# Optimization experiments

Hardware: AMD Instinct MI355X
Metric: run time of the kernel (lower is better)

Reference implementation:

```python
import jax, jax.numpy as jnp
import numpy as np

N_HEAD = 16
D_MODEL = 1024
D_HEAD = D_MODEL // N_HEAD  # 64
B, S = 1, 4096


def setup_inputs() -> dict:
    key = jax.random.key(0)
    ks = jax.random.split(key, 7)
    q = jax.random.normal(ks[0], (B, S, D_MODEL), dtype=jnp.float32)
    k = jax.random.normal(ks[1], (B, S, D_MODEL), dtype=jnp.float32)
    v = jax.random.normal(ks[2], (B, S, D_MODEL), dtype=jnp.float32)
    mask = jnp.ones((S, S), dtype=bool)
    # params match torch.rand init (uniform [0,1)); use uniform here too
    w_q = jax.random.uniform(ks[3], (D_MODEL, D_MODEL), dtype=jnp.float32)
    w_k = jax.random.uniform(ks[4], (D_HEAD, D_MODEL), dtype=jnp.float32)
    w_v = jax.random.uniform(ks[5], (D_HEAD, D_MODEL), dtype=jnp.float32)
    w_out = jax.random.uniform(ks[6], (D_MODEL, D_MODEL), dtype=jnp.float32)
    return {"q": q, "k": k, "v": v, "mask": mask,
            "w_q": w_q, "w_k": w_k, "w_v": w_v, "w_out": w_out}


def reference(q, k, v, mask, w_q, w_k, w_v, w_out):
    # F.linear(x, W) == x @ W.T
    query = q @ w_q.T                      # [b, n, d_model]
    key = k @ w_k.T                        # [b, s, d_head]  (single shared KV head)
    value = v @ w_v.T                      # [b, s, d_head]
    b, n, _ = query.shape
    query = query.reshape(b, n, N_HEAD, D_HEAD).transpose(0, 2, 1, 3)  # b h n d
    scores = jnp.einsum('bhnd,bsd->bhns', query, key) / jnp.sqrt(jnp.float32(D_HEAD))
    scores = jnp.where(mask[None, None], scores, jnp.float32(-jnp.inf))
    attn = jax.nn.softmax(scores, axis=-1)             # [b, h, n, s]
    out = jnp.einsum('bhns,bsd->bhnd', attn, value)    # [b, h, n, d]
    out = out.transpose(0, 2, 1, 3).reshape(b, n, D_MODEL)
    return out @ w_out.T
```

## Files before the change

### kernel.cpp

```cpp
#include <hip/hip_runtime.h>
#include <cstdint>
#include <cstddef>

#define S_LEN   4096
#define DM      1024
#define NHEAD   16
#define DH      64

typedef short bf16x8 __attribute__((ext_vector_type(8)));
typedef _Float16 f16x8 __attribute__((ext_vector_type(8)));
typedef float f32x4  __attribute__((ext_vector_type(4)));

__device__ __forceinline__ unsigned short f2bf(float x) {
    uint32_t u = __float_as_uint(x);
    u += 0x7fffu + ((u >> 16) & 1u);
    return (unsigned short)(u >> 16);
}
__device__ __forceinline__ float bf2f(unsigned short u) {
    return __uint_as_float(((uint32_t)u) << 16);
}
__device__ __forceinline__ unsigned short f2h(float x) {
    _Float16 h = (_Float16)x;
    return __builtin_bit_cast(unsigned short, h);
}
__device__ __forceinline__ unsigned pack_h2(float a, float b) {
    return __builtin_bit_cast(unsigned, __builtin_amdgcn_cvt_pkrtz(a, b));
}
__device__ __forceinline__ void gl_lds16(const unsigned short* g, unsigned short* l) {
    __builtin_amdgcn_global_load_lds(
        (const __attribute__((address_space(1))) unsigned int*)g,
        (__attribute__((address_space(3))) unsigned int*)l, 16, 0, 0);
}
__device__ __forceinline__ void split8(const float4& a0, const float4& a1,
                                       ushort4& h0, ushort4& h1,
                                       ushort4& l0, ushort4& l1) {
    h0.x = f2bf(a0.x); l0.x = f2bf(a0.x - bf2f(h0.x));
    h0.y = f2bf(a0.y); l0.y = f2bf(a0.y - bf2f(h0.y));
    h0.z = f2bf(a0.z); l0.z = f2bf(a0.z - bf2f(h0.z));
    h0.w = f2bf(a0.w); l0.w = f2bf(a0.w - bf2f(h0.w));
    h1.x = f2bf(a1.x); l1.x = f2bf(a1.x - bf2f(h1.x));
    h1.y = f2bf(a1.y); l1.y = f2bf(a1.y - bf2f(h1.y));
    h1.z = f2bf(a1.z); l1.z = f2bf(a1.z - bf2f(h1.z));
    h1.w = f2bf(a1.w); l1.w = f2bf(a1.w - bf2f(h1.w));
}

__launch_bounds__(256)
__global__ void pre_kernel(const float* __restrict__ kin, const float* __restrict__ vin,
                           const float* __restrict__ wk, const float* __restrict__ wv,
                           const float* __restrict__ q, const float* __restrict__ wq,
                           const float* __restrict__ wo,
                           unsigned short* __restrict__ Kf, unsigned short* __restrict__ Vtf,
                           unsigned short* __restrict__ qh, unsigned short* __restrict__ ql,
                           unsigned short* __restrict__ wqh, unsigned short* __restrict__ wql,
                           unsigned short* __restrict__ woh)
{
    __shared__ unsigned short As_h[64][72];
    __shared__ unsigned short Bs_h[64][72];
    __shared__ unsigned short As_l[64][72];
    __shared__ unsigned short Bs_l[64][72];

    const int tid = threadIdx.x;
    const int bx  = blockIdx.x;

    if (bx >= 128) {
        const int G1 = 1048576, GW = 262144;
        int i = (bx - 128) * 256 + tid;
        const float* src; unsigned short* h; unsigned short* l = nullptr; int off;
        if (i < G1)            { src = q;  h = qh;  l = ql;  off = i; }
        else if (i < G1 + GW)  { src = wq; h = wqh; l = wql; off = i - G1; }
        else                   { src = wo; h = woh;          off = i - G1 - GW; }
        float4 vv = reinterpret_cast<const float4*>(src)[off];
        ushort4 hh;
        hh.x = f2bf(vv.x); hh.y = f2bf(vv.y); hh.z = f2bf(vv.z); hh.w = f2bf(vv.w);
        reinterpret_cast<ushort4*>(h)[off] = hh;
        if (l) {
            ushort4 ll;
            ll.x = f2bf(vv.x - bf2f(hh.x)); ll.y = f2bf(vv.y - bf2f(hh.y));
            ll.z = f2bf(vv.z - bf2f(hh.z)); ll.w = f2bf(vv.w - bf2f(hh.w));
            reinterpret_cast<ushort4*>(l)[off] = ll;
        }
        return;
    }

    const int wave = tid >> 6;
    const int lane = tid & 63;
    const int lm   = lane & 15;
    const int quad = lane >> 4;
    const bool isK = (bx < 64);
    const int m0   = (bx & 63) * 64;
    const float* A = isK ? kin : vin;
    const float* B = isK ? wk : wv;

    f32x4 acc[4] = {};

    for (int kc = 0; kc < DM; kc += 64) {
        __syncthreads();
#pragma unroll
        for (int i = 0; i < 2; ++i) {
            int c   = tid + i * 256;
            int r   = c >> 3;
            int col = (c & 7) * 8;
            float4 a0 = *(const float4*)&A[(size_t)(m0 + r) * DM + kc + col];
            float4 a1 = *(const float4*)&A[(size_t)(m0 + r) * DM + kc + col + 4];
            float4 b0 = *(const float4*)&B[(size_t)r * DM + kc + col];
            float4 b1 = *(const float4*)&B[(size_t)r * DM + kc + col + 4];
            ushort4 h0, h1, l0, l1;
            split8(a0, a1, h0, h1, l0, l1);
            *(ushort4*)&As_h[r][col] = h0;  *(ushort4*)&As_h[r][col + 4] = h1;
            if (isK) { *(ushort4*)&As_l[r][col] = l0;  *(ushort4*)&As_l[r][col + 4] = l1; }
            split8(b0, b1, h0, h1, l0, l1);
            *(ushort4*)&Bs_h[r][col] = h0;  *(ushort4*)&Bs_h[r][col + 4] = h1;
            if (isK) { *(ushort4*)&Bs_l[r][col] = l0;  *(ushort4*)&Bs_l[r][col + 4] = l1; }
        }
        __syncthreads();
#pragma unroll
        for (int kk = 0; kk < 64; kk += 32) {
            bf16x8 bh = *(const bf16x8*)&Bs_h[wave * 16 + lm][kk + quad * 8];
            bf16x8 bl;
            if (isK) bl = *(const bf16x8*)&Bs_l[wave * 16 + lm][kk + quad * 8];
#pragma unroll
            for (int ms = 0; ms < 4; ++ms) {
                bf16x8 ah = *(const bf16x8*)&As_h[ms * 16 + lm][kk + quad * 8];
                acc[ms] = __builtin_amdgcn_mfma_f32_16x16x32_bf16(ah, bh, acc[ms], 0, 0, 0);
                if (isK) {
                    bf16x8 al = *(const bf16x8*)&As_l[ms * 16 + lm][kk + quad * 8];
                    acc[ms] = __builtin_amdgcn_mfma_f32_16x16x32_bf16(ah, bl, acc[ms], 0, 0, 0);
                    acc[ms] = __builtin_amdgcn_mfma_f32_16x16x32_bf16(al, bh, acc[ms], 0, 0, 0);
                }
            }
        }
    }

#pragma unroll
    for (int ms = 0; ms < 4; ++ms)
#pragma unroll
        for (int r = 0; r < 4; ++r) {
            int row = m0 + ms * 16 + quad * 4 + r;
            int col = wave * 16 + lm;
            if (isK) Kf[(size_t)row * DH + col] = f2h(acc[ms][r]);
            else     Vtf[(size_t)col * S_LEN + row] = f2h(acc[ms][r]);
        }
}

template<int TERMS, int MODE>
__launch_bounds__(256)
__global__ void gemm_big(const unsigned short* __restrict__ Ah,
                         const unsigned short* __restrict__ Al,
                         const unsigned short* __restrict__ Bh,
                         const unsigned short* __restrict__ Bl,
                         unsigned short* __restrict__ Ch,
                         float* __restrict__ Cf,
                         int M, int N, int K, int ldc)
{
    __shared__ unsigned short As_h[2][8192];
    __shared__ unsigned short Bs_h[2][8192];
    __shared__ unsigned short As_l[TERMS == 3 ? 2 : 1][TERMS == 3 ? 8192 : 1];
    __shared__ unsigned short Bs_l[TERMS == 3 ? 2 : 1][TERMS == 3 ? 8192 : 1];

    const int tid  = threadIdx.x;
    const int wave = tid >> 6;
    const int lane = tid & 63;
    const int lm   = lane & 15;
    const int quad = lane >> 4;
    const int wm   = wave >> 1;
    const int wn   = wave & 1;
    const int m0   = blockIdx.x * 128;
    const int n0   = blockIdx.y * 128;

    int srow[4], scol[4];
#pragma unroll
    for (int i = 0; i < 4; ++i) {
        int f = i * 256 + tid;
        srow[i] = f >> 3;
        scol[i] = ((f & 7) ^ (srow[i] & 7)) * 8;
    }

    auto stage = [&](int b, int kc) {
#pragma unroll
        for (int i = 0; i < 4; ++i) {
            const int dst = (i * 256 + wave * 64) * 8;
            gl_lds16(&Ah[(size_t)(m0 + srow[i]) * K + kc + scol[i]], &As_h[b][dst]);
            gl_lds16(&Bh[(size_t)(n0 + srow[i]) * K + kc + scol[i]], &Bs_h[b][dst]);
            if (TERMS == 3) {
                gl_lds16(&Al[(size_t)(m0 + srow[i]) * K + kc + scol[i]], &As_l[b][dst]);
                gl_lds16(&Bl[(size_t)(n0 + srow[i]) * K + kc + scol[i]], &Bs_l[b][dst]);
            }
        }
    };

    stage(0, 0);

    f32x4 acc[4][4] = {};
    const int nkc = K / 64;

    for (int it = 0; it < nkc; ++it) {
        const int b = it & 1;
        __syncthreads();
        if (it + 1 < nkc) stage(b ^ 1, (it + 1) * 64);

#pragma unroll
        for (int kk = 0; kk < 2; ++kk) {
            bf16x8 bh[4], bl[4];
#pragma unroll
            for (int ns = 0; ns < 4; ++ns) {
                const int off = (wn * 64 + ns * 16 + lm) * 64 + ((kk * 4 + quad) ^ (lm & 7)) * 8;
                bh[ns] = *(const bf16x8*)&Bs_h[b][off];
                if (TERMS == 3) bl[ns] = *(const bf16x8*)&Bs_l[b][off];
            }
#pragma unroll
            for (int ms = 0; ms < 4; ++ms) {
                const int off = (wm * 64 + ms * 16 + lm) * 64 + ((kk * 4 + quad) ^ (lm & 7)) * 8;
                bf16x8 ah = *(const bf16x8*)&As_h[b][off];
                bf16x8 al;
                if (TERMS == 3) al = *(const bf16x8*)&As_l[b][off];
#pragma unroll
                for (int ns = 0; ns < 4; ++ns) {
                    acc[ms][ns] = __builtin_amdgcn_mfma_f32_16x16x32_bf16(ah, bh[ns], acc[ms][ns], 0, 0, 0);
                    if (TERMS == 3) {
                        acc[ms][ns] = __builtin_amdgcn_mfma_f32_16x16x32_bf16(ah, bl[ns], acc[ms][ns], 0, 0, 0);
                        acc[ms][ns] = __builtin_amdgcn_mfma_f32_16x16x32_bf16(al, bh[ns], acc[ms][ns], 0, 0, 0);
                    }
                }
            }
        }
    }

#pragma unroll
    for (int ms = 0; ms < 4; ++ms)
#pragma unroll
        for (int ns = 0; ns < 4; ++ns)
#pragma unroll
            for (int r = 0; r < 4; ++r) {
                int row = m0 + wm * 64 + ms * 16 + quad * 4 + r;
                int col = n0 + wn * 64 + ns * 16 + lm;
                if (MODE == 2) Cf[(size_t)row * ldc + col] = acc[ms][ns][r];
                else           Ch[(size_t)row * ldc + col] = f2h(acc[ms][ns][r]);
            }
}

__launch_bounds__(128)
__global__ void flash_kernel(const unsigned short* __restrict__ Qf,
                             const unsigned short* __restrict__ Kf,
                             const unsigned short* __restrict__ Vt,
                             unsigned short* __restrict__ O)
{
    __shared__ unsigned short Ks[2][4096];
    __shared__ unsigned short Vs[2][4096];

    const int tid  = threadIdx.x;
    const int wave = tid >> 6;
    const int lane = tid & 63;
    const int lm   = lane & 15;
    const int quad = lane >> 4;
    const int q0   = blockIdx.x * 64;
    const int h    = blockIdx.y;
    const float c  = 0.125f * 1.44269504f;

    int srow[4], scol[4];
#pragma unroll
    for (int i = 0; i < 4; ++i) {
        int f = i * 128 + tid;
        srow[i] = f >> 3;
        scol[i] = ((f & 7) ^ (srow[i] & 7)) * 8;
    }

    auto stage = [&](int kt, int b) {
#pragma unroll
        for (int i = 0; i < 4; ++i) {
            const int dst = i * 1024 + wave * 512;
            gl_lds16(&Kf[(size_t)(kt + srow[i]) * DH + scol[i]], &Ks[b][dst]);
            gl_lds16(&Vt[(size_t)srow[i] * S_LEN + kt + scol[i]], &Vs[b][dst]);
        }
    };

    stage(0, 0);

    f16x8 qf[2][2];
#pragma unroll
    for (int nb = 0; nb < 2; ++nb)
#pragma unroll
        for (int kk = 0; kk < 2; ++kk) {
            size_t idx = (size_t)(q0 + wave * 32 + nb * 16 + lm) * DM + h * DH + kk * 32 + quad * 8;
            qf[nb][kk] = *(const f16x8*)&Qf[idx];
        }

    f32x4 oacc[2][4] = {};
    float m_run[2] = {-1e30f, -1e30f}, l_run[2] = {0.f, 0.f};

    for (int it = 0; it < 64; ++it) {
        const int b = it & 1;
        const int kt = it * 64;
        __syncthreads();
        if (it + 1 < 64) stage(kt + 64, b ^ 1);

        f32x4 sacc[2][4] = {};
#pragma unroll
        for (int kk = 0; kk < 2; ++kk) {
#pragma unroll
            for (int ms = 0; ms < 4; ++ms) {
                const int off = (ms * 16 + lm) * 64 + ((4 * kk + quad) ^ (lm & 7)) * 8;
                f16x8 kfr = *(const f16x8*)&Ks[b][off];
#pragma unroll
                for (int nb = 0; nb < 2; ++nb)
                    sacc[nb][ms] = __builtin_amdgcn_mfma_f32_16x16x32_f16(kfr, qf[nb][kk], sacc[nb][ms], 0, 0, 0);
            }
        }

        float mn[2];
#pragma unroll
        for (int nb = 0; nb < 2; ++nb) {
            float mx = -1e30f;
#pragma unroll
            for (int ms = 0; ms < 4; ++ms)
#pragma unroll
                for (int r = 0; r < 4; ++r) mx = fmaxf(mx, sacc[nb][ms][r]);
            mx = fmaxf(mx, __shfl_xor(mx, 16));
            mx = fmaxf(mx, __shfl_xor(mx, 32));
            mn[nb] = fmaxf(m_run[nb], mx);
        }

        if (__any((mn[0] > m_run[0]) || (mn[1] > m_run[1]))) {
#pragma unroll
            for (int mq = 0; mq < 2; ++mq) {
                float alpha = __builtin_amdgcn_exp2f((m_run[mq] - mn[mq]) * c);
                l_run[mq] *= alpha;
                m_run[mq] = mn[mq];
                float ar[4];
#pragma unroll
                for (int r = 0; r < 4; ++r) ar[r] = __shfl(alpha, quad * 4 + r);
#pragma unroll
                for (int nd = 0; nd < 4; ++nd)
#pragma unroll
                    for (int r = 0; r < 4; ++r) oacc[mq][nd][r] *= ar[r];
            }
        }

        unsigned pk[2][4][2];
#pragma unroll
        for (int nb = 0; nb < 2; ++nb) {
            float mc = m_run[nb] * c;
            float ps = 0.f;
#pragma unroll
            for (int ms = 0; ms < 4; ++ms) {
                float pr[4];
#pragma unroll
                for (int r = 0; r < 4; ++r) {
                    pr[r] = __builtin_amdgcn_exp2f(fmaf(sacc[nb][ms][r], c, -mc));
                    ps += pr[r];
                }
                pk[nb][ms][0] = pack_h2(pr[0], pr[1]);
                pk[nb][ms][1] = pack_h2(pr[2], pr[3]);
            }
            ps += __shfl_xor(ps, 16);
            ps += __shfl_xor(ps, 32);
            l_run[nb] += ps;
        }

#pragma unroll
        for (int kb = 0; kb < 2; ++kb) {
            f16x8 pa[2];
#pragma unroll
            for (int nb = 0; nb < 2; ++nb) {
                unsigned af[4] __attribute__((aligned(16)));
#pragma unroll
                for (int d = 0; d < 4; ++d) {
                    int srcl = ((2 * quad + (d >> 1)) & 3) * 16 + lm;
                    unsigned v_lo = (unsigned)__shfl((int)pk[nb][2 * kb][d & 1], srcl);
                    unsigned v_hi = (unsigned)__shfl((int)pk[nb][2 * kb + 1][d & 1], srcl);
                    af[d] = (quad < 2) ? v_lo : v_hi;
                }
                pa[nb] = *(f16x8*)af;
            }
#pragma unroll
            for (int nd = 0; nd < 4; ++nd) {
                const int off = (nd * 16 + lm) * 64 + ((4 * kb + quad) ^ (lm & 7)) * 8;
                f16x8 vb = *(const f16x8*)&Vs[b][off];
#pragma unroll
                for (int nb = 0; nb < 2; ++nb)
                    oacc[nb][nd] = __builtin_amdgcn_mfma_f32_16x16x32_f16(pa[nb], vb, oacc[nb][nd], 0, 0, 0);
            }
        }
    }

#pragma unroll
    for (int mq = 0; mq < 2; ++mq) {
        float lr[4];
#pragma unroll
        for (int r = 0; r < 4; ++r) lr[r] = 1.0f / __shfl(l_run[mq], quad * 4 + r);
#pragma unroll
        for (int nd = 0; nd < 4; ++nd)
#pragma unroll
            for (int r = 0; r < 4; ++r) {
                int qq = q0 + wave * 32 + mq * 16 + quad * 4 + r;
                O[(size_t)qq * DM + h * DH + nd * 16 + lm] = f2bf(oacc[mq][nd][r] * lr[r]);
            }
    }
}

extern "C" void kernel_launch(void* const* d_in, const int* in_sizes, int n_in,
                              void* d_out, int out_size, void* d_ws, size_t ws_size,
                              hipStream_t stream)
{
    (void)in_sizes; (void)n_in; (void)out_size; (void)ws_size;
    const float* q     = (const float*)d_in[0];
    const float* k     = (const float*)d_in[1];
    const float* v     = (const float*)d_in[2];
    const float* w_q   = (const float*)d_in[4];
    const float* w_k   = (const float*)d_in[5];
    const float* w_v   = (const float*)d_in[6];
    const float* w_out = (const float*)d_in[7];
    float* out = (float*)d_out;

    char* ws = (char*)d_ws;
    size_t off = 0;
    auto alloc = [&](size_t bytes) -> unsigned short* {
        unsigned short* p = (unsigned short*)(ws + off);
        off += (bytes + 255) & ~(size_t)255;
        return p;
    };
    const size_t SZ_QKV = (size_t)S_LEN * DM * 2;
    const size_t SZ_WQ  = (size_t)DM * DM * 2;
    const size_t SZ_KV  = (size_t)S_LEN * DH * 2;

    unsigned short* qh  = alloc(SZ_QKV);
    unsigned short* ql  = alloc(SZ_QKV);
    unsigned short* wqh = alloc(SZ_WQ);
    unsigned short* wql = alloc(SZ_WQ);
    unsigned short* woh = alloc(SZ_WQ);
    unsigned short* Qf  = alloc(SZ_QKV);
    unsigned short* Kf  = alloc(SZ_KV);
    unsigned short* Vtf = alloc(SZ_KV);
    unsigned short* Obf = alloc(SZ_QKV);

    pre_kernel<<<dim3(6272), 256, 0, stream>>>(k, v, w_k, w_v, q, w_q, w_out,
                                               Kf, Vtf, qh, ql, wqh, wql, woh);

    gemm_big<3, 3><<<dim3(32, 8), 256, 0, stream>>>(qh, ql, wqh, wql, Qf, nullptr,
                                                    S_LEN, DM, DM, DM);

    flash_kernel<<<dim3(64, 16), 128, 0, stream>>>(Qf, Kf, Vtf, Obf);

    gemm_big<1, 2><<<dim3(32, 8), 256, 0, stream>>>(Obf, nullptr, woh, nullptr, nullptr, out,
                                                    S_LEN, DM, DM, DM);
}
```

Measured before the change: 357.7 us.

## Double flash-attention tile to 128 queries and 128 keys per block

The flash kernel now runs 4 waves (256 threads) per block covering 128 query rows, and each iteration processes 128 keys instead of 64, halving both the grid and the iteration count. K and V tiles are staged into larger double-buffered LDS with a new 16-way XOR swizzle for the transposed V rows. This is meant to share each K/V tile across more queries and cut per-iteration sync and softmax-rescale overhead. In exchange it doubles LDS use and register pressure per wave (twice the score accumulators and packed P values), and leaves only 512 blocks, which may lower occupancy.

```diff
diff --git a/kernel.cpp b/kernel.cpp
--- a/kernel.cpp
+++ b/kernel.cpp
@@ -238,38 +238,39 @@
             }
 }
 
-__launch_bounds__(128)
+__launch_bounds__(256)
 __global__ void flash_kernel(const unsigned short* __restrict__ Qf,
                              const unsigned short* __restrict__ Kf,
                              const unsigned short* __restrict__ Vt,
                              unsigned short* __restrict__ O)
 {
-    __shared__ unsigned short Ks[2][4096];
-    __shared__ unsigned short Vs[2][4096];
+    __shared__ unsigned short Ks[2][8192];
+    __shared__ unsigned short Vs[2][8192];
 
     const int tid  = threadIdx.x;
     const int wave = tid >> 6;
     const int lane = tid & 63;
     const int lm   = lane & 15;
     const int quad = lane >> 4;
-    const int q0   = blockIdx.x * 64;
+    const int q0   = blockIdx.x * 128;
     const int h    = blockIdx.y;
+    const int NIT  = S_LEN / 128;
     const float c  = 0.125f * 1.44269504f;
 
-    int srow[4], scol[4];
+    int kr[4], kcol[4], vr[4], vcol[4];
 #pragma unroll
     for (int i = 0; i < 4; ++i) {
-        int f = i * 128 + tid;
-        srow[i] = f >> 3;
-        scol[i] = ((f & 7) ^ (srow[i] & 7)) * 8;
+        int f = i * 256 + tid;
+        kr[i] = f >> 3;  kcol[i] = ((f & 7) ^ (kr[i] & 7)) * 8;
+        vr[i] = f >> 4;  vcol[i] = ((f & 15) ^ (vr[i] & 15)) * 8;
     }
 
     auto stage = [&](int kt, int b) {
 #pragma unroll
         for (int i = 0; i < 4; ++i) {
-            const int dst = i * 1024 + wave * 512;
-            gl_lds16(&Kf[(size_t)(kt + srow[i]) * DH + scol[i]], &Ks[b][dst]);
-            gl_lds16(&Vt[(size_t)srow[i] * S_LEN + kt + scol[i]], &Vs[b][dst]);
+            const int dst = (i * 256 + wave * 64) * 8;
+            gl_lds16(&Kf[(size_t)(kt + kr[i]) * DH + kcol[i]], &Ks[b][dst]);
+            gl_lds16(&Vt[(size_t)vr[i] * S_LEN + kt + vcol[i]], &Vs[b][dst]);
         }
     };
 
@@ -287,33 +288,36 @@
     f32x4 oacc[2][4] = {};
     float m_run[2] = {-1e30f, -1e30f}, l_run[2] = {0.f, 0.f};
 
-    for (int it = 0; it < 64; ++it) {
+    for (int it = 0; it < NIT; ++it) {
         const int b = it & 1;
-        const int kt = it * 64;
+        const int kt = it * 128;
         __syncthreads();
-        if (it + 1 < 64) stage(kt + 64, b ^ 1);
-
-        f32x4 sacc[2][4] = {};
-#pragma unroll
-        for (int kk = 0; kk < 2; ++kk) {
-#pragma unroll
-            for (int ms = 0; ms < 4; ++ms) {
-                const int off = (ms * 16 + lm) * 64 + ((4 * kk + quad) ^ (lm & 7)) * 8;
-                f16x8 kfr = *(const f16x8*)&Ks[b][off];
-#pragma unroll
-                for (int nb = 0; nb < 2; ++nb)
-                    sacc[nb][ms] = __builtin_amdgcn_mfma_f32_16x16x32_f16(kfr, qf[nb][kk], sacc[nb][ms], 0, 0, 0);
-            }
-        }
+        if (it + 1 < NIT) stage(kt + 128, b ^ 1);
+
+        f32x4 sacc[2][2][4] = {};
+#pragma unroll
+        for (int t = 0; t < 2; ++t)
+#pragma unroll
+            for (int kk = 0; kk < 2; ++kk)
+#pragma unroll
+                for (int ms = 0; ms < 4; ++ms) {
+                    const int off = (t * 64 + ms * 16 + lm) * 64 + ((4 * kk + quad) ^ (lm & 7)) * 8;
+                    f16x8 kfr = *(const f16x8*)&Ks[b][off];
+#pragma unroll
+                    for (int nb = 0; nb < 2; ++nb)
+                        sacc[nb][t][ms] = __builtin_amdgcn_mfma_f32_16x16x32_f16(kfr, qf[nb][kk], sacc[nb][t][ms], 0, 0, 0);
+                }
 
         float mn[2];
 #pragma unroll
         for (int nb = 0; nb < 2; ++nb) {
             float mx = -1e30f;
 #pragma unroll
-            for (int ms = 0; ms < 4; ++ms)
-#pragma unroll
-                for (int r = 0; r < 4; ++r) mx = fmaxf(mx, sacc[nb][ms][r]);
+            for (int t = 0; t < 2; ++t)
+#pragma unroll
+                for (int ms = 0; ms < 4; ++ms)
+#pragma unroll
+                    for (int r = 0; r < 4; ++r) mx = fmaxf(mx, sacc[nb][t][ms][r]);
             mx = fmaxf(mx, __shfl_xor(mx, 16));
             mx = fmaxf(mx, __shfl_xor(mx, 32));
             mn[nb] = fmaxf(m_run[nb], mx);
@@ -335,51 +339,56 @@
             }
         }
 
-        unsigned pk[2][4][2];
+        unsigned pk[2][2][4][2];
 #pragma unroll
         for (int nb = 0; nb < 2; ++nb) {
             float mc = m_run[nb] * c;
             float ps = 0.f;
 #pragma unroll
-            for (int ms = 0; ms < 4; ++ms) {
-                float pr[4];
-#pragma unroll
-                for (int r = 0; r < 4; ++r) {
-                    pr[r] = __builtin_amdgcn_exp2f(fmaf(sacc[nb][ms][r], c, -mc));
-                    ps += pr[r];
-                }
-                pk[nb][ms][0] = pack_h2(pr[0], pr[1]);
-                pk[nb][ms][1] = pack_h2(pr[2], pr[3]);
-            }
+            for (int t = 0; t < 2; ++t)
+#pragma unroll
+                for (int ms = 0; ms < 4; ++ms) {
+                    float pr[4];
+#pragma unroll
+                    for (int r = 0; r < 4; ++r) {
+                        pr[r] = __builtin_amdgcn_exp2f(fmaf(sacc[nb][t][ms][r], c, -mc));
+                        ps += pr[r];
+                    }
+                    pk[nb][t][ms][0] = pack_h2(pr[0], pr[1]);
+                    pk[nb][t][ms][1] = pack_h2(pr[2], pr[3]);
+                }
             ps += __shfl_xor(ps, 16);
             ps += __shfl_xor(ps, 32);
             l_run[nb] += ps;
         }
 
 #pragma unroll
-        for (int kb = 0; kb < 2; ++kb) {
-            f16x8 pa[2];
-#pragma unroll
-            for (int nb = 0; nb < 2; ++nb) {
-                unsigned af[4] __attribute__((aligned(16)));
-#pragma unroll
-                for (int d = 0; d < 4; ++d) {
-                    int srcl = ((2 * quad + (d >> 1)) & 3) * 16 + lm;
-                    unsigned v_lo = (unsigned)__shfl((int)pk[nb][2 * kb][d & 1], srcl);
-                    unsigned v_hi = (unsigned)__shfl((int)pk[nb][2 * kb + 1][d & 1], srcl);
-                    af[d] = (quad < 2) ? v_lo : v_hi;
-                }
-                pa[nb] = *(f16x8*)af;
-            }
-#pragma unroll
-            for (int nd = 0; nd < 4; ++nd) {
-                const int off = (nd * 16 + lm) * 64 + ((4 * kb + quad) ^ (lm & 7)) * 8;
-                f16x8 vb = *(const f16x8*)&Vs[b][off];
-#pragma unroll
-                for (int nb = 0; nb < 2; ++nb)
-                    oacc[nb][nd] = __builtin_amdgcn_mfma_f32_16x16x32_f16(pa[nb], vb, oacc[nb][nd], 0, 0, 0);
-            }
-        }
+        for (int t = 0; t < 2; ++t)
+#pragma unroll
+            for (int kb = 0; kb < 2; ++kb) {
+                f16x8 pa[2];
+#pragma unroll
+                for (int nb = 0; nb < 2; ++nb) {
+                    unsigned af[4] __attribute__((aligned(16)));
+#pragma unroll
+                    for (int d = 0; d < 4; ++d) {
+                        int srcl = ((2 * quad + (d >> 1)) & 3) * 16 + lm;
+                        unsigned v_lo = (unsigned)__shfl((int)pk[nb][t][2 * kb][d & 1], srcl);
+                        unsigned v_hi = (unsigned)__shfl((int)pk[nb][t][2 * kb + 1][d & 1], srcl);
+                        af[d] = (quad < 2) ? v_lo : v_hi;
+                    }
+                    pa[nb] = *(f16x8*)af;
+                }
+                const int kbg = t * 2 + kb;
+#pragma unroll
+                for (int nd = 0; nd < 4; ++nd) {
+                    const int off = (nd * 16 + lm) * 128 + (((kbg * 4 + quad) ^ lm) * 8);
+                    f16x8 vb = *(const f16x8*)&Vs[b][off];
+#pragma unroll
+                    for (int nb = 0; nb < 2; ++nb)
+                        oacc[nb][nd] = __builtin_amdgcn_mfma_f32_16x16x32_f16(pa[nb], vb, oacc[nb][nd], 0, 0, 0);
+                }
+            }
     }
 
 #pragma unroll
@@ -438,7 +447,7 @@
     gemm_big<3, 3><<<dim3(32, 8), 256, 0, stream>>>(qh, ql, wqh, wql, Qf, nullptr,
                                                     S_LEN, DM, DM, DM);
 
-    flash_kernel<<<dim3(64, 16), 128, 0, stream>>>(Qf, Kf, Vtf, Obf);
+    flash_kernel<<<dim3(32, 16), 256, 0, stream>>>(Qf, Kf, Vtf, Obf);
 
     gemm_big<1, 2><<<dim3(32, 8), 256, 0, stream>>>(Obf, nullptr, woh, nullptr, nullptr, out,
                                                     S_LEN, DM, DM, DM);
```

Measured after the change: 340.6 us. -4.8%, faster.
